# Kernel optimization log

Measured on AMD Instinct MI355X. Metric: run time of the kernel, lower is better.

## Reference

```python
import jax, jax.numpy as jnp
import numpy as np

NUM_HEADS = 16
HEAD_DIM = 128  # d_out // num_heads
D_IN = 2048
D_OUT = 2048
B = 2
T = 2048
W_SCALE = 0.02  # keep softmax logits in a sane range


def setup_inputs() -> dict:
    key = jax.random.key(0)
    ks = jax.random.split(key, 6)
    x = jax.random.normal(ks[0], (B, T, D_IN), dtype=jnp.float32)
    Wq = jax.random.normal(ks[1], (D_OUT, D_IN), dtype=jnp.float32) * W_SCALE
    Wk = jax.random.normal(ks[2], (HEAD_DIM, D_IN), dtype=jnp.float32) * W_SCALE
    Wv = jax.random.normal(ks[3], (HEAD_DIM, D_IN), dtype=jnp.float32) * W_SCALE
    Wo = jax.random.normal(ks[4], (D_OUT, D_OUT), dtype=jnp.float32) * W_SCALE
    bo = jnp.zeros((D_OUT,), dtype=jnp.float32)
    return {"x": x, "Wq": Wq, "Wk": Wk, "Wv": Wv, "Wo": Wo, "bo": bo}


def reference(x, Wq, Wk, Wv, Wo, bo):
    b, t, _ = x.shape
    # projections (torch nn.Linear: y = x @ W.T)
    q = jnp.einsum('btd,ed->bte', x, Wq).reshape(b, t, NUM_HEADS, HEAD_DIM)
    q = q.transpose(0, 2, 1, 3)                      # [b, H, T, hd]
    k = jnp.einsum('btd,ed->bte', x, Wk)             # [b, T, hd] single KV head
    v = jnp.einsum('btd,ed->bte', x, Wv)             # [b, T, hd]
    # MQA: single K/V head broadcast across all query heads
    scale = 1.0 / jnp.sqrt(jnp.float32(HEAD_DIM))
    scores = jnp.einsum('bhqd,bkd->bhqk', q, k) * scale  # [b, H, T, T]
    # NOTE: the original module computes a causal mask but never applies it,
    # so attention is unmasked (faithful to source).
    w = jax.nn.softmax(scores, axis=-1)
    ctx = jnp.einsum('bhqk,bkd->bhqd', w, v)         # [b, H, T, hd]
    ctx = ctx.transpose(0, 2, 1, 3).reshape(b, t, D_OUT)
    return jnp.einsum('btd,ed->bte', ctx, Wo) + bo
```

## Files before the change

### kernel.cpp

```cpp
#include <hip/hip_runtime.h>

typedef unsigned short u16;
typedef unsigned int   u32;
typedef __bf16 bf16x8 __attribute__((ext_vector_type(8)));
typedef float  f32x4  __attribute__((ext_vector_type(4)));
typedef u32    u32x2  __attribute__((ext_vector_type(2)));

constexpr int TB   = 2;
constexpr int TT   = 2048;
constexpr int DIN  = 2048;
constexpr int DOUT = 2048;
constexpr int NH   = 16;
constexpr int HD   = 128;
constexpr int MR   = TB * TT;
constexpr int NQKV = DOUT + 2 * HD;

constexpr float QSC = 0.08838834764831845f * 1.4426950408889634f;

__device__ __forceinline__ u16 f2b(float f) {
  return __builtin_bit_cast(u16, (__bf16)f);
}

__global__ __launch_bounds__(256) void k_cast_all(const float* __restrict__ x,
                                                  const float* __restrict__ wq,
                                                  const float* __restrict__ wk,
                                                  const float* __restrict__ wv,
                                                  const float* __restrict__ wo,
                                                  u16* __restrict__ xb,
                                                  u16* __restrict__ wqkv,
                                                  u16* __restrict__ wob) {
  int bid = blockIdx.x;
  const float* s; u16* d; int base;
  if (bid < 8192)       { s = x;  d = xb;   base = bid; }
  else if (bid < 12288) { s = wq; d = wqkv; base = bid - 8192; }
  else if (bid < 12544) { s = wk; d = wqkv + (size_t)DOUT * DIN;        base = bid - 12288; }
  else if (bid < 12800) { s = wv; d = wqkv + (size_t)(DOUT + HD) * DIN; base = bid - 12544; }
  else                  { s = wo; d = wob;  base = bid - 12800; }
  int i = (base * 256 + threadIdx.x) * 4;
  float4 v = *(const float4*)(s + i);
  ushort4 o;
  o.x = f2b(v.x); o.y = f2b(v.y); o.z = f2b(v.z); o.w = f2b(v.w);
  *(ushort4*)(d + i) = o;
}

__device__ __forceinline__ void async16(const u16* g, u16* l) {
  __builtin_amdgcn_global_load_lds((const __attribute__((address_space(1))) void*)g,
                                   (__attribute__((address_space(3))) void*)l,
                                   16, 0, 0);
}

#define GPH3(SUB, BUFI, STAGE_STMT, WAIT_STMT)                                 \
  {                                                                            \
    bf16x8 af[4], bfv[4];                                                      \
    const char* baA = (const char*)&lA[BUFI][0];                               \
    const char* baB = (const char*)&lB[BUFI][0];                               \
    const int cso = (((SUB) * 4 + kq) ^ sw) << 4;                              \
    _Pragma("unroll")                                                          \
    for (int mm = 0; mm < 4; ++mm)                                             \
      af[mm] = *(const bf16x8*)(baA + (wr * 64 + mm * 16 + r16) * 128 + cso);  \
    _Pragma("unroll")                                                          \
    for (int n = 0; n < 4; ++n)                                                \
      bfv[n] = *(const bf16x8*)(baB + (wc * 64 + n * 16 + r16) * 128 + cso);   \
    STAGE_STMT;                                                                \
    __builtin_amdgcn_s_barrier();                                              \
    __builtin_amdgcn_s_setprio(1);                                             \
    _Pragma("unroll")                                                          \
    for (int mm = 0; mm < 4; ++mm)                                             \
      _Pragma("unroll")                                                        \
      for (int n = 0; n < 4; ++n)                                              \
        acc[mm][n] = __builtin_amdgcn_mfma_f32_16x16x32_bf16(                  \
            af[mm], bfv[n], acc[mm][n], 0, 0, 0);                              \
    __builtin_amdgcn_s_setprio(0);                                             \
    WAIT_STMT;                                                                 \
    __builtin_amdgcn_s_barrier();                                              \
  }

template<bool F32OUT>
__global__ __launch_bounds__(512) void k_gemm8(const u16* __restrict__ A,
                                               const u16* __restrict__ Bm,
                                               void* __restrict__ Cv,
                                               const float* __restrict__ bias,
                                               int M, int N, int K) {
  __shared__ u16 lA[3][128 * 64];
  __shared__ u16 lB[3][256 * 64];
  const int tid = threadIdx.x;
  const int w = tid >> 6, l = tid & 63;
  const int wr = w >> 2, wc = w & 3;
  const int r16 = l & 15, kq = l >> 4;
  const int sw = r16 & 7;

  int nwg = gridDim.x * gridDim.y;
  int wg = blockIdx.y * gridDim.x + blockIdx.x;
  if ((nwg & 7) == 0) wg = (wg & 7) * (nwg >> 3) + (wg >> 3);
  const int rowS = (wg / gridDim.x) * 128, colS = (wg % gridDim.x) * 256;

  auto stageA2 = [&](int buf, int k0) {
#pragma unroll
    for (int i = 0; i < 2; ++i) {
      int e = i * 512 + tid;
      int row = e >> 3;
      int gc = ((e & 7) ^ (row & 7)) * 8;
      async16(A + (size_t)(rowS + row) * K + k0 + gc, &lA[buf][e * 8]);
    }
  };
  auto stageB = [&](int buf, int k0, int i0, int i1) {
#pragma unroll
    for (int i = 0; i < 4; ++i) {
      if (i < i0 || i >= i1) continue;
      int e = i * 512 + tid;
      int row = e >> 3;
      int gc = ((e & 7) ^ (row & 7)) * 8;
      async16(Bm + (size_t)(colS + row) * K + k0 + gc, &lB[buf][e * 8]);
    }
  };

  f32x4 acc[4][4] = {};

  stageA2(0, 0);
  stageB(0, 0, 0, 4);
  stageA2(1, 64);
  stageB(1, 64, 0, 4);
  asm volatile("s_waitcnt vmcnt(6)" ::: "memory");
  __builtin_amdgcn_s_barrier();

  const int NT = K >> 6;
  for (int t = 0; t < NT; ++t) {
    const int bi = t % 3;
    const int sb = (t + 2) % 3;
    const bool st = (t + 2 < NT);
    const int k2 = (t + 2) << 6;

    GPH3(0, bi,
         { if (st) { stageA2(sb, k2); stageB(sb, k2, 0, 1); } },
         {});
    GPH3(1, bi,
         { if (st) { stageB(sb, k2, 1, 4); } },
         {
           if (t + 1 < NT) {
             if (st) asm volatile("s_waitcnt vmcnt(6)" ::: "memory");
             else    asm volatile("s_waitcnt vmcnt(0)" ::: "memory");
           }
         });
  }

#pragma unroll
  for (int m = 0; m < 4; ++m)
#pragma unroll
    for (int n = 0; n < 4; ++n)
#pragma unroll
      for (int j = 0; j < 4; ++j) {
        int r = rowS + wr * 64 + m * 16 + kq * 4 + j;
        int c = colS + wc * 64 + n * 16 + r16;
        if constexpr (F32OUT) {
          ((float*)Cv)[(size_t)r * N + c] = acc[m][n][j] + bias[c];
        } else {
          float v = acc[m][n][j];
          if (c < DOUT) v *= QSC;
          ((u16*)Cv)[(size_t)r * N + c] = f2b(v);
        }
      }
}

__global__ __launch_bounds__(256) void k_transpose_v(const u16* __restrict__ qkv,
                                                     u16* __restrict__ vtg) {
  __shared__ u16 tile[64 * 136];
  const int blk = blockIdx.x;
  const int b = blk / (TT / 64), t0 = (blk % (TT / 64)) * 64;
  const int tid = threadIdx.x;
#pragma unroll
  for (int i = 0; i < 4; ++i) {
    int e = i * 256 + tid;
    int row = e >> 4, col = (e & 15) * 8;
    *(uint4*)&tile[row * 136 + col] =
        *(const uint4*)(qkv + (size_t)(b * TT + t0 + row) * NQKV + DOUT + HD + col);
  }
  __syncthreads();
#pragma unroll
  for (int i = 0; i < 4; ++i) {
    int e = i * 256 + tid;
    int d = e >> 3, tc = (e & 7) * 8;
    u16 tmp[8];
#pragma unroll
    for (int j = 0; j < 8; ++j) tmp[j] = tile[(tc + j) * 136 + d];
    *(uint4*)(vtg + ((size_t)b * HD + d) * TT + t0 + tc) = *(uint4*)tmp;
  }
}

#define KT_IDX(r, c) ((r) * 128 + ((c) ^ (((r) & 7) << 3)))
#define VT_IDX(r, c) ((r) * 64 + ((c) ^ (((r) & 7) << 3)))

__global__ __launch_bounds__(512) void k_attn(const u16* __restrict__ qkv,
                                              const u16* __restrict__ vtg,
                                              u16* __restrict__ ctxg) {
  __shared__ u16 Kt[2][64 * 128];
  __shared__ u16 Vt[2][128 * 64];
  __shared__ u16 Pt[8][16 * 40];

  const int qt = blockIdx.x, h = blockIdx.y, b = blockIdx.z;
  const int tid = threadIdx.x, w = tid >> 6, l = tid & 63;
  const int r16 = l & 15, kq = l >> 4;
  const int q0 = qt * 128 + w * 16;
  const size_t rowbase = (size_t)b * TT;

  bf16x8 qf[4];
  const u16* qrow = qkv + (rowbase + q0 + r16) * NQKV + h * HD + kq * 8;
#pragma unroll
  for (int kk = 0; kk < 4; ++kk) qf[kk] = *(const bf16x8*)(qrow + kk * 32);

  const int krow0 = tid >> 4, kcol = (tid & 15) * 8;
  const int vrow0 = tid >> 3, vcol = (tid & 7) * 8;
  const u16* kglob = qkv + (rowbase)*NQKV + DOUT;
  const u16* vglob = vtg + (size_t)b * HD * TT;

  uint4 kr0, kr1, vr0, vr1;
  auto load_tiles = [&](int kv0) {
    const u16* kb = kglob + (size_t)kv0 * NQKV;
    kr0 = *(const uint4*)(kb + (size_t)krow0 * NQKV + kcol);
    kr1 = *(const uint4*)(kb + (size_t)(krow0 + 32) * NQKV + kcol);
    const u16* vb = vglob + kv0;
    vr0 = *(const uint4*)(vb + (size_t)vrow0 * TT + vcol);
    vr1 = *(const uint4*)(vb + (size_t)(vrow0 + 64) * TT + vcol);
  };
  auto write_tiles = [&](int buf) {
    *(uint4*)&Kt[buf][KT_IDX(krow0, kcol)]      = kr0;
    *(uint4*)&Kt[buf][KT_IDX(krow0 + 32, kcol)] = kr1;
    *(uint4*)&Vt[buf][VT_IDX(vrow0, vcol)]      = vr0;
    *(uint4*)&Vt[buf][VT_IDX(vrow0 + 64, vcol)] = vr1;
  };

  f32x4 ctx[8] = {};
  float l_run = 0.0f;

  load_tiles(0);
  write_tiles(0);
  __syncthreads();

  for (int t = 0; t < TT / 64; ++t) {
    const int cur = t & 1;
    if (t < TT / 64 - 1) load_tiles((t + 1) * 64);

    f32x4 s[4] = {};
#pragma unroll
    for (int n = 0; n < 4; ++n) {
      bf16x8 kf[4];
#pragma unroll
      for (int kk = 0; kk < 4; ++kk)
        kf[kk] = *(const bf16x8*)&Kt[cur][KT_IDX(n * 16 + r16, kk * 32 + kq * 8)];
      __builtin_amdgcn_s_setprio(1);
#pragma unroll
      for (int kk = 0; kk < 4; ++kk)
        s[n] = __builtin_amdgcn_mfma_f32_16x16x32_bf16(kf[kk], qf[kk], s[n], 0, 0, 0);
      __builtin_amdgcn_s_setprio(0);
    }

    float rsum = 0.0f;
    float p[4][4];
#pragma unroll
    for (int n = 0; n < 4; ++n)
#pragma unroll
      for (int j = 0; j < 4; ++j) {
        p[n][j] = exp2f(s[n][j]);
        rsum += p[n][j];
      }
    rsum += __shfl_xor(rsum, 16);
    rsum += __shfl_xor(rsum, 32);
    l_run += rsum;

    u32 pk[4][2];
#pragma unroll
    for (int n = 0; n < 4; ++n) {
      pk[n][0] = (u32)f2b(p[n][0]) | ((u32)f2b(p[n][1]) << 16);
      pk[n][1] = (u32)f2b(p[n][2]) | ((u32)f2b(p[n][3]) << 16);
    }

    u16* pw = Pt[w];
#pragma unroll
    for (int hh = 0; hh < 2; ++hh) {
      u32x2 w0, w1;
      w0[0] = pk[2 * hh][0];     w0[1] = pk[2 * hh][1];
      w1[0] = pk[2 * hh + 1][0]; w1[1] = pk[2 * hh + 1][1];
      *(u32x2*)&pw[r16 * 40 + kq * 4]      = w0;
      *(u32x2*)&pw[r16 * 40 + 16 + kq * 4] = w1;
      bf16x8 pf = *(const bf16x8*)&pw[r16 * 40 + kq * 8];
      __builtin_amdgcn_s_setprio(1);
#pragma unroll
      for (int f = 0; f < 8; ++f) {
        bf16x8 vf = *(const bf16x8*)&Vt[cur][VT_IDX(f * 16 + r16, hh * 32 + kq * 8)];
        ctx[f] = __builtin_amdgcn_mfma_f32_16x16x32_bf16(vf, pf, ctx[f], 0, 0, 0);
      }
      __builtin_amdgcn_s_setprio(0);
    }

    if (t < TT / 64 - 1) write_tiles(cur ^ 1);
    __syncthreads();
  }

  const float inv = 1.0f / l_run;
  u16* crow = ctxg + (rowbase + q0 + r16) * DOUT + h * HD + kq * 4;
#pragma unroll
  for (int f = 0; f < 8; ++f) {
    u32x2 o;
    o[0] = (u32)f2b(ctx[f][0] * inv) | ((u32)f2b(ctx[f][1] * inv) << 16);
    o[1] = (u32)f2b(ctx[f][2] * inv) | ((u32)f2b(ctx[f][3] * inv) << 16);
    *(u32x2*)(crow + f * 16) = o;
  }
}

extern "C" void kernel_launch(void* const* d_in, const int* in_sizes, int n_in,
                              void* d_out, int out_size, void* d_ws, size_t ws_size,
                              hipStream_t stream) {
  const float* x  = (const float*)d_in[0];
  const float* Wq = (const float*)d_in[1];
  const float* Wk = (const float*)d_in[2];
  const float* Wv = (const float*)d_in[3];
  const float* Wo = (const float*)d_in[4];
  const float* bo = (const float*)d_in[5];
  float* out = (float*)d_out;

  char* ws = (char*)d_ws;
  u16* xb   = (u16*)(ws + 0);
  u16* wqkv = (u16*)(ws + 16777216);
  u16* wo   = (u16*)(ws + 26214400);
  u16* qkv  = (u16*)(ws + 34603008);
  u16* vtg  = (u16*)(ws + 53477376);
  u16* ctx  = (u16*)(ws + 54525952);

  k_cast_all<<<16896, 256, 0, stream>>>(x, Wq, Wk, Wv, Wo, xb, wqkv, wo);

  k_gemm8<false><<<dim3(NQKV / 256, MR / 128), 512, 0, stream>>>(
      xb, wqkv, (void*)qkv, nullptr, MR, NQKV, DIN);

  k_transpose_v<<<TB * TT / 64, 256, 0, stream>>>(qkv, vtg);

  k_attn<<<dim3(TT / 128, NH, TB), 512, 0, stream>>>(qkv, vtg, ctx);

  k_gemm8<true><<<dim3(DOUT / 256, MR / 128), 512, 0, stream>>>(
      ctx, wo, (void*)out, bo, MR, DOUT, DOUT);
}
```

Baseline: 317.1 us.

## Process two 16-row query tiles per wave in attention to reuse K/V fragments

Each wave in the attention kernel now handles 32 query rows (two 16-row tiles) instead of 16, so a block covers 256 queries and the grid halves. K and V fragments read from LDS, and the K/V tiles loaded from global memory, are reused across twice as many queries, which lowers LDS and global traffic per unit of MFMA work. The cost is roughly double the accumulator and Q-fragment registers, which may reduce occupancy, plus only 256 blocks in the grid, which may underfill the GPU.

```diff
diff --git a/kernel.cpp b/kernel.cpp
--- a/kernel.cpp
+++ b/kernel.cpp
@@ -194,18 +194,21 @@
                                               u16* __restrict__ ctxg) {
   __shared__ u16 Kt[2][64 * 128];
   __shared__ u16 Vt[2][128 * 64];
-  __shared__ u16 Pt[8][16 * 40];
+  __shared__ u16 Pt[8][2][16 * 40];
 
   const int qt = blockIdx.x, h = blockIdx.y, b = blockIdx.z;
   const int tid = threadIdx.x, w = tid >> 6, l = tid & 63;
   const int r16 = l & 15, kq = l >> 4;
-  const int q0 = qt * 128 + w * 16;
+  const int q0 = qt * 256 + w * 32;
   const size_t rowbase = (size_t)b * TT;
 
-  bf16x8 qf[4];
-  const u16* qrow = qkv + (rowbase + q0 + r16) * NQKV + h * HD + kq * 8;
-#pragma unroll
-  for (int kk = 0; kk < 4; ++kk) qf[kk] = *(const bf16x8*)(qrow + kk * 32);
+  bf16x8 qf[2][4];
+#pragma unroll
+  for (int qi = 0; qi < 2; ++qi) {
+    const u16* qrow = qkv + (rowbase + q0 + qi * 16 + r16) * NQKV + h * HD + kq * 8;
+#pragma unroll
+    for (int kk = 0; kk < 4; ++kk) qf[qi][kk] = *(const bf16x8*)(qrow + kk * 32);
+  }
 
   const int krow0 = tid >> 4, kcol = (tid & 15) * 8;
   const int vrow0 = tid >> 3, vcol = (tid & 7) * 8;
@@ -228,8 +231,8 @@
     *(uint4*)&Vt[buf][VT_IDX(vrow0 + 64, vcol)] = vr1;
   };
 
-  f32x4 ctx[8] = {};
-  float l_run = 0.0f;
+  f32x4 ctx0[8] = {}, ctx1[8] = {};
+  float l_run0 = 0.0f, l_run1 = 0.0f;
 
   load_tiles(0);
   write_tiles(0);
@@ -239,7 +242,7 @@
     const int cur = t & 1;
     if (t < TT / 64 - 1) load_tiles((t + 1) * 64);
 
-    f32x4 s[4] = {};
+    f32x4 s0[4] = {}, s1[4] = {};
 #pragma unroll
     for (int n = 0; n < 4; ++n) {
       bf16x8 kf[4];
@@ -248,45 +251,66 @@
         kf[kk] = *(const bf16x8*)&Kt[cur][KT_IDX(n * 16 + r16, kk * 32 + kq * 8)];
       __builtin_amdgcn_s_setprio(1);
 #pragma unroll
-      for (int kk = 0; kk < 4; ++kk)
-        s[n] = __builtin_amdgcn_mfma_f32_16x16x32_bf16(kf[kk], qf[kk], s[n], 0, 0, 0);
+      for (int kk = 0; kk < 4; ++kk) {
+        s0[n] = __builtin_amdgcn_mfma_f32_16x16x32_bf16(kf[kk], qf[0][kk], s0[n], 0, 0, 0);
+        s1[n] = __builtin_amdgcn_mfma_f32_16x16x32_bf16(kf[kk], qf[1][kk], s1[n], 0, 0, 0);
+      }
       __builtin_amdgcn_s_setprio(0);
     }
 
-    float rsum = 0.0f;
-    float p[4][4];
-#pragma unroll
-    for (int n = 0; n < 4; ++n)
-#pragma unroll
-      for (int j = 0; j < 4; ++j) {
-        p[n][j] = exp2f(s[n][j]);
-        rsum += p[n][j];
-      }
-    rsum += __shfl_xor(rsum, 16);
-    rsum += __shfl_xor(rsum, 32);
-    l_run += rsum;
-
-    u32 pk[4][2];
-#pragma unroll
-    for (int n = 0; n < 4; ++n) {
-      pk[n][0] = (u32)f2b(p[n][0]) | ((u32)f2b(p[n][1]) << 16);
-      pk[n][1] = (u32)f2b(p[n][2]) | ((u32)f2b(p[n][3]) << 16);
-    }
-
-    u16* pw = Pt[w];
+    u32 pk0[4][2], pk1[4][2];
+    {
+      float rsum = 0.0f;
+#pragma unroll
+      for (int n = 0; n < 4; ++n) {
+        float pa = exp2f(s0[n][0]), pb = exp2f(s0[n][1]);
+        float pc = exp2f(s0[n][2]), pd = exp2f(s0[n][3]);
+        rsum += (pa + pb) + (pc + pd);
+        pk0[n][0] = (u32)f2b(pa) | ((u32)f2b(pb) << 16);
+        pk0[n][1] = (u32)f2b(pc) | ((u32)f2b(pd) << 16);
+      }
+      rsum += __shfl_xor(rsum, 16);
+      rsum += __shfl_xor(rsum, 32);
+      l_run0 += rsum;
+    }
+    {
+      float rsum = 0.0f;
+#pragma unroll
+      for (int n = 0; n < 4; ++n) {
+        float pa = exp2f(s1[n][0]), pb = exp2f(s1[n][1]);
+        float pc = exp2f(s1[n][2]), pd = exp2f(s1[n][3]);
+        rsum += (pa + pb) + (pc + pd);
+        pk1[n][0] = (u32)f2b(pa) | ((u32)f2b(pb) << 16);
+        pk1[n][1] = (u32)f2b(pc) | ((u32)f2b(pd) << 16);
+      }
+      rsum += __shfl_xor(rsum, 16);
+      rsum += __shfl_xor(rsum, 32);
+      l_run1 += rsum;
+    }
+
 #pragma unroll
     for (int hh = 0; hh < 2; ++hh) {
-      u32x2 w0, w1;
-      w0[0] = pk[2 * hh][0];     w0[1] = pk[2 * hh][1];
-      w1[0] = pk[2 * hh + 1][0]; w1[1] = pk[2 * hh + 1][1];
-      *(u32x2*)&pw[r16 * 40 + kq * 4]      = w0;
-      *(u32x2*)&pw[r16 * 40 + 16 + kq * 4] = w1;
-      bf16x8 pf = *(const bf16x8*)&pw[r16 * 40 + kq * 8];
+      u16* pw0 = Pt[w][0];
+      u16* pw1 = Pt[w][1];
+      {
+        u32x2 a0, a1, b0, b1;
+        a0[0] = pk0[2 * hh][0];     a0[1] = pk0[2 * hh][1];
+        a1[0] = pk0[2 * hh + 1][0]; a1[1] = pk0[2 * hh + 1][1];
+        b0[0] = pk1[2 * hh][0];     b0[1] = pk1[2 * hh][1];
+        b1[0] = pk1[2 * hh + 1][0]; b1[1] = pk1[2 * hh + 1][1];
+        *(u32x2*)&pw0[r16 * 40 + kq * 4]      = a0;
+        *(u32x2*)&pw0[r16 * 40 + 16 + kq * 4] = a1;
+        *(u32x2*)&pw1[r16 * 40 + kq * 4]      = b0;
+        *(u32x2*)&pw1[r16 * 40 + 16 + kq * 4] = b1;
+      }
+      bf16x8 pf0 = *(const bf16x8*)&pw0[r16 * 40 + kq * 8];
+      bf16x8 pf1 = *(const bf16x8*)&pw1[r16 * 40 + kq * 8];
       __builtin_amdgcn_s_setprio(1);
 #pragma unroll
       for (int f = 0; f < 8; ++f) {
         bf16x8 vf = *(const bf16x8*)&Vt[cur][VT_IDX(f * 16 + r16, hh * 32 + kq * 8)];
-        ctx[f] = __builtin_amdgcn_mfma_f32_16x16x32_bf16(vf, pf, ctx[f], 0, 0, 0);
+        ctx0[f] = __builtin_amdgcn_mfma_f32_16x16x32_bf16(vf, pf0, ctx0[f], 0, 0, 0);
+        ctx1[f] = __builtin_amdgcn_mfma_f32_16x16x32_bf16(vf, pf1, ctx1[f], 0, 0, 0);
       }
       __builtin_amdgcn_s_setprio(0);
     }
@@ -295,14 +319,27 @@
     __syncthreads();
   }
 
-  const float inv = 1.0f / l_run;
-  u16* crow = ctxg + (rowbase + q0 + r16) * DOUT + h * HD + kq * 4;
-#pragma unroll
-  for (int f = 0; f < 8; ++f) {
-    u32x2 o;
-    o[0] = (u32)f2b(ctx[f][0] * inv) | ((u32)f2b(ctx[f][1] * inv) << 16);
-    o[1] = (u32)f2b(ctx[f][2] * inv) | ((u32)f2b(ctx[f][3] * inv) << 16);
-    *(u32x2*)(crow + f * 16) = o;
+  {
+    const float inv = 1.0f / l_run0;
+    u16* crow = ctxg + (rowbase + q0 + r16) * DOUT + h * HD + kq * 4;
+#pragma unroll
+    for (int f = 0; f < 8; ++f) {
+      u32x2 o;
+      o[0] = (u32)f2b(ctx0[f][0] * inv) | ((u32)f2b(ctx0[f][1] * inv) << 16);
+      o[1] = (u32)f2b(ctx0[f][2] * inv) | ((u32)f2b(ctx0[f][3] * inv) << 16);
+      *(u32x2*)(crow + f * 16) = o;
+    }
+  }
+  {
+    const float inv = 1.0f / l_run1;
+    u16* crow = ctxg + (rowbase + q0 + 16 + r16) * DOUT + h * HD + kq * 4;
+#pragma unroll
+    for (int f = 0; f < 8; ++f) {
+      u32x2 o;
+      o[0] = (u32)f2b(ctx1[f][0] * inv) | ((u32)f2b(ctx1[f][1] * inv) << 16);
+      o[1] = (u32)f2b(ctx1[f][2] * inv) | ((u32)f2b(ctx1[f][3] * inv) << 16);
+      *(u32x2*)(crow + f * 16) = o;
+    }
   }
 }
 
@@ -332,7 +369,7 @@
 
   k_transpose_v<<<TB * TT / 64, 256, 0, stream>>>(qkv, vtg);
 
-  k_attn<<<dim3(TT / 128, NH, TB), 512, 0, stream>>>(qkv, vtg, ctx);
+  k_attn<<<dim3(TT / 256, NH, TB), 512, 0, stream>>>(qkv, vtg, ctx);
 
   k_gemm8<true><<<dim3(DOUT / 256, MR / 128), 512, 0, stream>>>(
       ctx, wo, (void*)out, bo, MR, DOUT, DOUT);
```

Result: no change. 313.3 us (-1.2%).
